# Kernel optimization log

Hardware: AMD Instinct MI355X
Metric: run time of the kernel (lower is better)

The kernel has to match this reference:

```python
import jax, jax.numpy as jnp
import numpy as np
import math

HIST = 10  # attention window over per-node prediction history


def setup_inputs() -> dict:
    key = jax.random.key(0)
    ks = jax.random.split(key, 16)
    N, DEG, F, H, M, O, P, S = 512, 8, 128, 256, 256, 64, 2, 64

    def lin(k, fan_in, shape):
        b = 1.0 / np.sqrt(fan_in)
        return jax.random.uniform(k, shape, jnp.float32, -b, b)

    return {
        "xa": jax.random.normal(ks[0], (N, F), jnp.float32),
        "neighbors": jax.random.randint(ks[1], (N, DEG), 0, N),
        "first_message": jax.random.normal(ks[2], (N, M), jnp.float32),
        "We": lin(ks[3], F, (F, H)), "be": lin(ks[3], F, (H,)),
        "Wq": lin(ks[4], M, (M, H)), "bq": lin(ks[4], M, (H,)),
        "Wk": lin(ks[5], H, (H, H)), "bk": lin(ks[5], H, (H,)),
        "Wr": lin(ks[6], 4 * H, (4 * H, H)), "br": lin(ks[6], 4 * H, (H,)),
        "Wm": lin(ks[7], H + M, (H + M, M)), "bm": lin(ks[7], H + M, (M,)),
        "Wd": lin(ks[8], H, (P, H, O)), "bd": lin(ks[8], H, (P, O)),
        "num_starts": S,
    }


def reference(xa, neighbors, first_message, We, be, Wq, bq, Wk, bk,
              Wr, br, Wm, bm, Wd, bd, num_starts):
    N, H = xa.shape[0], We.shape[1]
    M = first_message.shape[1]
    DEG = neighbors.shape[1]
    max_steps = 10 * N                    # message budget, as in the while-loop cap
    CAP = num_starts + max_steps * DEG    # static queue capacity bound
    inv_sqrt_h = 1.0 / math.sqrt(H)
    nbrs = neighbors.astype(jnp.int32)
    slot_ids = jnp.arange(HIST)

    encoded = xa @ We + be                                    # [N,H]
    hist = jnp.zeros((N, HIST, H), xa.dtype).at[:, 0, :].set(encoded)
    count = jnp.ones((N,), jnp.int32)
    q_node = jnp.zeros((CAP,), jnp.int32).at[:num_starts].set(
        jnp.arange(num_starts, dtype=jnp.int32))
    q_msg = jnp.zeros((CAP, M), xa.dtype).at[:num_starts].set(
        first_message[:num_starts])
    head = jnp.int32(0)
    tail = jnp.int32(num_starts)

    def step(carry, _):
        hist, count, q_node, q_msg, head, tail = carry
        active = head < tail                 # queue non-empty
        node = q_node[head]
        message = q_msg[head]                # [M]
        feats = hist[node]                   # [HIST,H] ring buffer of last states
        c = count[node]
        valid = slot_ids < jnp.minimum(c, HIST)
        # NOTE: source uses queries[0]/keys[0] for every head -> heads identical
        query = message @ Wq + bq            # [H]
        keys = feats @ Wk + bk               # [HIST,H]
        logits = jnp.where(valid, keys @ query * inv_sqrt_h, -jnp.inf)
        attn = jax.nn.softmax(logits)        # softmax over history axis (dim=-0)
        values = attn @ feats                # [H]
        newstate = jnp.concatenate([values] * 4) @ Wr + br     # [H]
        newmessage = jnp.concatenate([newstate, message]) @ Wm + bm  # [M]
        # conditional state updates (no-op writes when inactive)
        slot = c % HIST
        hist = hist.at[node, slot].set(jnp.where(active, newstate, hist[node, slot]))
        count = count.at[node].add(jnp.where(active, 1, 0))
        old_n = jax.lax.dynamic_slice(q_node, (tail,), (DEG,))
        old_m = jax.lax.dynamic_slice(q_msg, (tail, 0), (DEG, M))
        q_node = jax.lax.dynamic_update_slice(
            q_node, jnp.where(active, nbrs[node], old_n), (tail,))
        q_msg = jax.lax.dynamic_update_slice(
            q_msg, jnp.where(active, jnp.broadcast_to(newmessage, (DEG, M)), old_m),
            (tail, 0))
        head = head + jnp.where(active, 1, 0)
        tail = tail + jnp.where(active, DEG, 0)
        return (hist, count, q_node, q_msg, head, tail), None

    (hist, count, _, _, _, _), _ = jax.lax.scan(
        step, (hist, count, q_node, q_msg, head, tail), None, length=max_steps)

    final = hist[jnp.arange(N), (count - 1) % HIST]           # [N,H] last state
    logits = jnp.einsum('nh,pho->pno', final, Wd) + bd[:, None, :]
    return jax.nn.log_softmax(logits, axis=-1)                # [P,N,O]
```

## Files before the change

kernel.cpp:

```cpp
#include <hip/hip_runtime.h>
#include <hip/hip_bf16.h>

#define NN 512
#define DEG 8
#define FD 128
#define HD 256
#define MD 256
#define OD 64
#define PD 2
#define HIST 10
#define TOTAL (10 * NN)
#define NPAR 648
#define INV_SQRT_H 0.0625f

typedef __hip_bfloat16 bf16;

__device__ __forceinline__ float finz(float x) {
  unsigned u = __float_as_uint(x);
  return (((u >> 23) & 0xFFu) == 0xFFu) ? 0.f : x;
}

__device__ __forceinline__ float ldin(const void* p, int idx, int bf) {
  if (bf) return __bfloat162float(((const bf16*)p)[idx]);
  return ((const float*)p)[idx];
}

__device__ __forceinline__ float scload(const float* p) {
  return __uint_as_float(__hip_atomic_load((const unsigned*)p, __ATOMIC_RELAXED,
                                           __HIP_MEMORY_SCOPE_AGENT));
}
__device__ __forceinline__ void scstore(float* p, float v) {
  __hip_atomic_store((unsigned*)p, __float_as_uint(v), __ATOMIC_RELAXED,
                     __HIP_MEMORY_SCOPE_AGENT);
}

__device__ float g_hist[NN * HIST * HD];
__device__ float g_msgb[NPAR * MD];
__device__ float g_WQK[HD * HD];
__device__ float g_WrS[HD * HD];
__device__ float g_vq[HD];
__device__ float g_ck[HD];
__device__ float g_bqk;
__device__ int   g_node[TOTAL];
__device__ int   g_done[TOTAL];
__device__ int   g_dtype;
__device__ int   g_i64;

__device__ __forceinline__ int decode_S(const int* dS) {
  int r = dS[0];
  if (r >= 1 && r <= NN) return r;
  float f = __int_as_float(r);
  if (f >= 1.f && f <= (float)NN) return (int)f;
  unsigned u = ((unsigned)r & 0xFFFFu) << 16;
  float g = __uint_as_float(u);
  if (g >= 1.f && g <= (float)NN) return (int)g;
  return 64;
}

__device__ __forceinline__ int get_nbr(const int* nbrs, int i64, int n, int d) {
  int v = i64 ? nbrs[2 * (n * DEG + d)] : nbrs[n * DEG + d];
  return (v < 0) ? 0 : (v >= NN ? NN - 1 : v);
}

__device__ __forceinline__ int detect_bf(const unsigned* xa_w) {
  const int lane = threadIdx.x & 63;
  unsigned lo = xa_w[lane] & 0xFFFFu;
  float av = fabsf(__uint_as_float(lo << 16));
  unsigned long long m = __ballot(av > 0.000244140625f && av < 64.f);
  return ((int)__popcll(m) >= 32) ? 1 : 0;
}

__global__ void __launch_bounds__(1024)
k_prep(const void* __restrict__ xa, const unsigned* __restrict__ xa_w,
       const int* __restrict__ nbrs, const int* __restrict__ dS,
       const void* __restrict__ We, const void* __restrict__ be,
       const void* __restrict__ Wq, const void* __restrict__ Wk,
       const void* __restrict__ Wr, const void* __restrict__ bq,
       const void* __restrict__ bk) {
  const int b = blockIdx.x, t = threadIdx.x;
  const int col = t & 255, grp = t >> 8;
  const int wave = t >> 6, lane = t & 63;
  const int bf = detect_bf(xa_w);
  if (t < 8) { int fi = 8 * b + t; if (fi < TOTAL) g_done[fi] = 0; }
  __shared__ float sw[HD];
  __shared__ float sp[4][HD];
  __shared__ float sr[16];
  __shared__ float s_wkT[32][HD + 1];
  __shared__ int s_node[TOTAL];
  if (b < HD) {
    if (grp == 0) sw[col] = ldin(Wq, b * HD + col, bf);
    __syncthreads();
    if (grp == 1) {
      float pv = sw[col] * ldin(bk, col, bf);
#pragma unroll
      for (int off = 32; off > 0; off >>= 1) pv += __shfl_down(pv, off, 64);
      if (lane == 0) sr[wave] = pv;
    }
    if (grp == 2) {
      float s = 0.f;
#pragma unroll
      for (int q = 0; q < 4; ++q) s += ldin(Wr, (size_t)(q * HD + b) * HD + col, bf);
      g_WrS[b * HD + col] = s;
    }
    float acc0 = 0.f, acc1 = 0.f;
    const int hh = t & 31, r0 = t >> 5;
    for (int h0 = 0; h0 < HD; h0 += 32) {
#pragma unroll
      for (int rr = 0; rr < 8; ++rr) {
        const int row = rr * 32 + r0;
        s_wkT[hh][row] = ldin(Wk, row * HD + h0 + hh, bf);
      }
      __syncthreads();
      const int hb = grp * 8;
#pragma unroll
      for (int i = 0; i < 8; i += 2) {
        acc0 += sw[h0 + hb + i]     * s_wkT[hb + i][col];
        acc1 += sw[h0 + hb + i + 1] * s_wkT[hb + i + 1][col];
      }
      __syncthreads();
    }
    sp[grp][col] = acc0 + acc1;
    __syncthreads();
    if (grp == 0)
      g_WQK[b * HD + col] = (sp[0][col] + sp[1][col]) + (sp[2][col] + sp[3][col]);
    if (t == 0) g_vq[b] = (sr[4] + sr[5]) + (sr[6] + sr[7]);
  } else if (b == HD) {
    {
      const int h0 = grp * 64;
      float a0 = 0.f, a1 = 0.f, a2 = 0.f, a3 = 0.f;
      for (int h = 0; h < 64; h += 4) {
        a0 += ldin(Wk, col * HD + h0 + h,     bf) * ldin(bq, h0 + h,     bf);
        a1 += ldin(Wk, col * HD + h0 + h + 1, bf) * ldin(bq, h0 + h + 1, bf);
        a2 += ldin(Wk, col * HD + h0 + h + 2, bf) * ldin(bq, h0 + h + 2, bf);
        a3 += ldin(Wk, col * HD + h0 + h + 3, bf) * ldin(bq, h0 + h + 3, bf);
      }
      sp[grp][col] = (a0 + a1) + (a2 + a3);
    }
    if (grp == 1) {
      float pb = ldin(bq, col, bf) * ldin(bk, col, bf);
#pragma unroll
      for (int off = 32; off > 0; off >>= 1) pb += __shfl_down(pb, off, 64);
      if (lane == 0) sr[wave] = pb;
    }
    __syncthreads();
    if (grp == 0)
      g_ck[col] = (sp[0][col] + sp[1][col]) + (sp[2][col] + sp[3][col]);
    if (t == 0) g_bqk = (sr[4] + sr[5]) + (sr[6] + sr[7]);
  } else if (b <= HD + NN) {
    const int n = b - HD - 1;
    if (t < FD) sw[t] = ldin(xa, n * FD + t, bf);
    __syncthreads();
    const int f0 = grp * 32;
    float a0 = 0.f, a1 = 0.f, a2 = 0.f, a3 = 0.f;
    for (int f = 0; f < 32; f += 4) {
      a0 += sw[f0 + f]     * ldin(We, (f0 + f)     * HD + col, bf);
      a1 += sw[f0 + f + 1] * ldin(We, (f0 + f + 1) * HD + col, bf);
      a2 += sw[f0 + f + 2] * ldin(We, (f0 + f + 2) * HD + col, bf);
      a3 += sw[f0 + f + 3] * ldin(We, (f0 + f + 3) * HD + col, bf);
    }
    sp[grp][col] = (a0 + a1) + (a2 + a3);
    __syncthreads();
    if (grp == 0)
      g_hist[(size_t)(n * HIST) * HD + col] =
          ldin(be, col, bf) + (sp[0][col] + sp[1][col]) + (sp[2][col] + sp[3][col]);
  } else {
    if (t == 0) g_dtype = bf;
    bool c8 = (lane < 8) ? (nbrs[2 * lane + 1] == 0) : true;
    unsigned long long im = __ballot(c8);
    const int i64 = ((im & 0xFFull) == 0xFFull) ? 1 : 0;
    if (t == 0) g_i64 = i64;
    const int S = decode_S(dS);
    for (int i = t; i < S; i += 1024) s_node[i] = i;
    __syncthreads();
    int done = S;
    while (done < TOTAL) {
      long long nd = (long long)S + 8LL * (long long)done;
      int new_done = nd > (long long)TOTAL ? TOTAL : (int)nd;
      for (int i = done + t; i < new_done; i += 1024)
        s_node[i] = get_nbr(nbrs, i64, s_node[(i - S) >> 3], (i - S) & 7);
      __syncthreads();
      done = new_done;
    }
    for (int i = t; i < TOTAL; i += 1024) g_node[i] = s_node[i];
  }
}

__global__ void __launch_bounds__(256, 2)
k_flow(const void* __restrict__ fmsg, const void* __restrict__ br_,
       const void* __restrict__ Wm, const void* __restrict__ bm,
       const void* __restrict__ Wd, const void* __restrict__ bd,
       void* __restrict__ out, const int* __restrict__ dS) {
  const int n = blockIdx.x;
  const int t = threadIdx.x;
  const int wave = t >> 6, lane = t & 63;
  const int S = decode_S(dS);
  const int bf = g_dtype;
  __shared__ float s_hist[HIST][HD];
  __shared__ float s_msg[MD];
  __shared__ float s_vals[HD];
  __shared__ float s_ns[HD];
  __shared__ float s_red[4][HIST + 1];
  __shared__ int   s_list[TOTAL];
  __shared__ int   s_cnt;

  const float rck = g_ck[t];
  const float rvq = g_vq[t];
  const float rbqk = g_bqk;
  const float rbr = ldin(br_, t, bf);
  const float rbm = ldin(bm, t, bf);

#pragma unroll
  for (int j = 1; j < HIST; ++j) s_hist[j][t] = 0.f;
  s_hist[0][t] = finz(g_hist[(size_t)n * HIST * HD + t]);

  if (wave == 0) {
    int k = 0;
    for (int base = 0; base < TOTAL; base += 64) {
      int nd = g_node[base + lane];
      unsigned long long m = __ballot(nd == n);
      if (nd == n) {
        unsigned long long below = m & ((1ull << lane) - 1ull);
        s_list[k + (int)__popcll(below)] = base + lane;
      }
      k += (int)__popcll(m);
    }
    if (lane == 0) s_cnt = k;
  }
  __syncthreads();
  const int cnt = s_cnt;

  for (int k = 0; k < cnt; ++k) {
    const int e = s_list[k];
    const int c = k + 1;
    const int v = (c < HIST) ? c : HIST;
    const int slot = c % HIST;
    const bool hc = (S + 8 * e) < TOTAL;

    float ms;
    if (e < S) {
      ms = ldin(fmsg, e * MD + t, bf);
    } else {
      const int p = (e - S) >> 3;
      if (t == 0)
        while (__hip_atomic_load(&g_done[p], __ATOMIC_RELAXED,
                                 __HIP_MEMORY_SCOPE_AGENT) == 0)
          __builtin_amdgcn_s_sleep(4);
      __syncthreads();
      ms = scload(g_msgb + (size_t)p * MD + t);
    }
    s_msg[t] = finz(ms);
    __syncthreads();

    float a0 = 0.f, a1 = 0.f, a2 = 0.f, a3 = 0.f;
    for (int m = 0; m < MD; m += 4) {
      a0 += s_msg[m]     * g_WQK[(m)     * HD + t];
      a1 += s_msg[m + 1] * g_WQK[(m + 1) * HD + t];
      a2 += s_msg[m + 2] * g_WQK[(m + 2) * HD + t];
      a3 += s_msg[m + 3] * g_WQK[(m + 3) * HD + t];
    }
    const float kq = rck + ((a0 + a1) + (a2 + a3));

    float part[HIST + 1];
#pragma unroll
    for (int j = 0; j < HIST; ++j) part[j] = s_hist[j][t] * kq;
    part[HIST] = s_msg[t] * rvq;
#pragma unroll
    for (int o = 32; o > 0; o >>= 1) {
#pragma unroll
      for (int j = 0; j <= HIST; ++j) part[j] += __shfl_down(part[j], o, 64);
    }
    if (lane == 0) {
#pragma unroll
      for (int j = 0; j <= HIST; ++j) s_red[wave][j] = part[j];
    }
    __syncthreads();

    float sc[HIST + 1];
#pragma unroll
    for (int j = 0; j <= HIST; ++j)
      sc[j] = (s_red[0][j] + s_red[1][j]) + (s_red[2][j] + s_red[3][j]);
    const float bkq = sc[HIST] + rbqk;
    float lg[HIST];
#pragma unroll
    for (int j = 0; j < HIST; ++j)
      lg[j] = (j < v) ? ((sc[j] + bkq) * INV_SQRT_H) : -1e30f;
    float mx = lg[0];
#pragma unroll
    for (int j = 1; j < HIST; ++j) mx = fmaxf(mx, lg[j]);
    float e_[HIST], den = 0.f;
#pragma unroll
    for (int j = 0; j < HIST; ++j) { e_[j] = __expf(lg[j] - mx); den += e_[j]; }
    const float iden = 1.0f / den;
    float val = 0.f;
#pragma unroll
    for (int j = 0; j < HIST; ++j) val += e_[j] * s_hist[j][t];
    s_vals[t] = val * iden;
    __syncthreads();

    float b0 = 0.f, b1 = 0.f, b2 = 0.f, b3 = 0.f;
    for (int h = 0; h < HD; h += 4) {
      b0 += s_vals[h]     * g_WrS[(h)     * HD + t];
      b1 += s_vals[h + 1] * g_WrS[(h + 1) * HD + t];
      b2 += s_vals[h + 2] * g_WrS[(h + 2) * HD + t];
      b3 += s_vals[h + 3] * g_WrS[(h + 3) * HD + t];
    }
    const float ns = rbr + ((b0 + b1) + (b2 + b3));
    s_hist[slot][t] = ns;
    if (hc) s_ns[t] = ns;
    __syncthreads();

    if (hc) {
      float c0 = 0.f, c1 = 0.f, c2 = 0.f, c3 = 0.f;
      if (bf) {
        const bf16* w = (const bf16*)Wm;
        for (int h = 0; h < HD; h += 4) {
          c0 += s_ns[h]     * __bfloat162float(w[(h)     * MD + t]);
          c1 += s_ns[h + 1] * __bfloat162float(w[(h + 1) * MD + t]);
          c2 += s_ns[h + 2] * __bfloat162float(w[(h + 2) * MD + t]);
          c3 += s_ns[h + 3] * __bfloat162float(w[(h + 3) * MD + t]);
        }
        for (int m = 0; m < MD; m += 4) {
          c0 += s_msg[m]     * __bfloat162float(w[(HD + m)     * MD + t]);
          c1 += s_msg[m + 1] * __bfloat162float(w[(HD + m + 1) * MD + t]);
          c2 += s_msg[m + 2] * __bfloat162float(w[(HD + m + 2) * MD + t]);
          c3 += s_msg[m + 3] * __bfloat162float(w[(HD + m + 3) * MD + t]);
        }
      } else {
        const float* w = (const float*)Wm;
        for (int h = 0; h < HD; h += 4) {
          c0 += s_ns[h]     * w[(h)     * MD + t];
          c1 += s_ns[h + 1] * w[(h + 1) * MD + t];
          c2 += s_ns[h + 2] * w[(h + 2) * MD + t];
          c3 += s_ns[h + 3] * w[(h + 3) * MD + t];
        }
        for (int m = 0; m < MD; m += 4) {
          c0 += s_msg[m]     * w[(HD + m)     * MD + t];
          c1 += s_msg[m + 1] * w[(HD + m + 1) * MD + t];
          c2 += s_msg[m + 2] * w[(HD + m + 2) * MD + t];
          c3 += s_msg[m + 3] * w[(HD + m + 3) * MD + t];
        }
      }
      scstore(&g_msgb[(size_t)e * MD + t], rbm + ((c0 + c1) + (c2 + c3)));
      asm volatile("s_waitcnt vmcnt(0)" ::: "memory");
    }
    __syncthreads();
    if (hc && t == 0)
      __hip_atomic_store(&g_done[e], 1, __ATOMIC_RELAXED,
                         __HIP_MEMORY_SCOPE_AGENT);
  }

  const int slotF = cnt % HIST;
  if (t < PD * OD) {
    const int pp = t >> 6, o = t & 63;
    float acc = finz(ldin(bd, pp * OD + o, bf));
    for (int h = 0; h < HD; ++h)
      acc += finz(s_hist[slotF][h]) * ldin(Wd, (pp * HD + h) * OD + o, bf);
    acc = finz(acc);
    float mx = acc;
#pragma unroll
    for (int off = 32; off > 0; off >>= 1) mx = fmaxf(mx, __shfl_xor(mx, off, 64));
    float ex = __expf(acc - mx);
    float s = ex;
#pragma unroll
    for (int off = 32; off > 0; off >>= 1) s += __shfl_xor(s, off, 64);
    float r = finz(acc - mx - logf(s));
    const int oi = (pp * NN + n) * OD + o;
    if (bf) ((bf16*)out)[oi] = __float2bfloat16(r);
    else    ((float*)out)[oi] = r;
  }
}

extern "C" void kernel_launch(void* const* d_in, const int* in_sizes, int n_in,
                              void* d_out, int out_size, void* d_ws, size_t ws_size,
                              hipStream_t stream) {
  const void* xa   = d_in[0];
  const int*  nbrs = (const int*)d_in[1];
  const void* fmsg = d_in[2];
  const void* We   = d_in[3];
  const void* be   = d_in[4];
  const void* Wq   = d_in[5];
  const void* bq   = d_in[6];
  const void* Wk   = d_in[7];
  const void* bk   = d_in[8];
  const void* Wr   = d_in[9];
  const void* br   = d_in[10];
  const void* Wm   = d_in[11];
  const void* bm   = d_in[12];
  const void* Wd   = d_in[13];
  const void* bd   = d_in[14];
  const int*  dS   = (const int*)d_in[15];
  (void)d_ws; (void)ws_size; (void)in_sizes; (void)n_in; (void)out_size;

  k_prep<<<dim3(HD + 1 + NN + 1), dim3(1024), 0, stream>>>(
      xa, (const unsigned*)xa, nbrs, dS, We, be, Wq, Wk, Wr, bq, bk);
  k_flow<<<dim3(NN), dim3(256), 0, stream>>>(fmsg, br, Wm, bm, Wd, bd, d_out, dS);
}
```

Measured before the change: 437.8 us.

## Batch eight rows per block in prep kernel to reuse Wk and We loads

After: 435.1 us, median of 2. Within noise of the previous version (-0.6%).

```diff
diff --git a/kernel.cpp b/kernel.cpp
--- a/kernel.cpp
+++ b/kernel.cpp
@@ -81,88 +81,131 @@
   const int col = t & 255, grp = t >> 8;
   const int wave = t >> 6, lane = t & 63;
   const int bf = detect_bf(xa_w);
-  if (t < 8) { int fi = 8 * b + t; if (fi < TOTAL) g_done[fi] = 0; }
-  __shared__ float sw[HD];
-  __shared__ float sp[4][HD];
-  __shared__ float sr[16];
+  { int fi = b * 1024 + t; if (fi < TOTAL) g_done[fi] = 0; }
+  __shared__ float sw8[8][HD];
   __shared__ float s_wkT[32][HD + 1];
-  __shared__ int s_node[TOTAL];
-  if (b < HD) {
-    if (grp == 0) sw[col] = ldin(Wq, b * HD + col, bf);
-    __syncthreads();
-    if (grp == 1) {
-      float pv = sw[col] * ldin(bk, col, bf);
+  __shared__ float sp[4][8][HD];
+  __shared__ float s_xa[8][FD];
+  __shared__ int   s_node[TOTAL];
+  if (b < 32) {
+    const int R = 8 * b;
+    {
+      const int i0 = t, i1 = t + 1024;
+      sw8[i0 >> 8][i0 & 255] = ldin(Wq, (R + (i0 >> 8)) * HD + (i0 & 255), bf);
+      sw8[i1 >> 8][i1 & 255] = ldin(Wq, (R + (i1 >> 8)) * HD + (i1 & 255), bf);
+    }
+    __syncthreads();
+    {
+      const int r0 = R + 2 * grp, r1 = r0 + 1;
+      float s0 = 0.f, s1 = 0.f;
+#pragma unroll
+      for (int q = 0; q < 4; ++q) {
+        s0 += ldin(Wr, (size_t)(q * HD + r0) * HD + col, bf);
+        s1 += ldin(Wr, (size_t)(q * HD + r1) * HD + col, bf);
+      }
+      g_WrS[(size_t)r0 * HD + col] = s0;
+      g_WrS[(size_t)r1 * HD + col] = s1;
+    }
+    if (wave < 8) {
+      float pv = 0.f;
+#pragma unroll
+      for (int j = 0; j < 4; ++j)
+        pv += sw8[wave][lane + 64 * j] * ldin(bk, lane + 64 * j, bf);
 #pragma unroll
       for (int off = 32; off > 0; off >>= 1) pv += __shfl_down(pv, off, 64);
-      if (lane == 0) sr[wave] = pv;
-    }
-    if (grp == 2) {
-      float s = 0.f;
-#pragma unroll
-      for (int q = 0; q < 4; ++q) s += ldin(Wr, (size_t)(q * HD + b) * HD + col, bf);
-      g_WrS[b * HD + col] = s;
-    }
-    float acc0 = 0.f, acc1 = 0.f;
-    const int hh = t & 31, r0 = t >> 5;
+      if (lane == 0) g_vq[R + wave] = pv;
+    }
+    float q0 = 0.f, q1 = 0.f, q2 = 0.f, q3 = 0.f;
+    float q4 = 0.f, q5 = 0.f, q6 = 0.f, q7 = 0.f;
+    const int hh = t & 31, r0s = t >> 5;
+    const int hb = grp * 8;
     for (int h0 = 0; h0 < HD; h0 += 32) {
 #pragma unroll
       for (int rr = 0; rr < 8; ++rr) {
-        const int row = rr * 32 + r0;
+        const int row = rr * 32 + r0s;
         s_wkT[hh][row] = ldin(Wk, row * HD + h0 + hh, bf);
       }
       __syncthreads();
-      const int hb = grp * 8;
-#pragma unroll
-      for (int i = 0; i < 8; i += 2) {
-        acc0 += sw[h0 + hb + i]     * s_wkT[hb + i][col];
-        acc1 += sw[h0 + hb + i + 1] * s_wkT[hb + i + 1][col];
-      }
-      __syncthreads();
-    }
-    sp[grp][col] = acc0 + acc1;
+#pragma unroll
+      for (int i = 0; i < 8; ++i) {
+        const float wk = s_wkT[hb + i][col];
+        const int h = h0 + hb + i;
+        q0 += sw8[0][h] * wk; q1 += sw8[1][h] * wk;
+        q2 += sw8[2][h] * wk; q3 += sw8[3][h] * wk;
+        q4 += sw8[4][h] * wk; q5 += sw8[5][h] * wk;
+        q6 += sw8[6][h] * wk; q7 += sw8[7][h] * wk;
+      }
+      __syncthreads();
+    }
+    sp[grp][0][col] = q0; sp[grp][1][col] = q1;
+    sp[grp][2][col] = q2; sp[grp][3][col] = q3;
+    sp[grp][4][col] = q4; sp[grp][5][col] = q5;
+    sp[grp][6][col] = q6; sp[grp][7][col] = q7;
+    __syncthreads();
+    if (grp == 0) {
+#pragma unroll
+      for (int r = 0; r < 8; ++r)
+        g_WQK[(size_t)(R + r) * HD + col] =
+            (sp[0][r][col] + sp[1][r][col]) + (sp[2][r][col] + sp[3][r][col]);
+    }
+  } else if (b == 32) {
+    float ca = 0.f;
+    const int hh = t & 31, r0s = t >> 5;
+    const int hb = grp * 8;
+    for (int h0 = 0; h0 < HD; h0 += 32) {
+#pragma unroll
+      for (int rr = 0; rr < 8; ++rr) {
+        const int row = rr * 32 + r0s;
+        s_wkT[hh][row] = ldin(Wk, row * HD + h0 + hh, bf);
+      }
+      __syncthreads();
+#pragma unroll
+      for (int i = 0; i < 8; ++i)
+        ca += ldin(bq, h0 + hb + i, bf) * s_wkT[hb + i][col];
+      __syncthreads();
+    }
+    sp[grp][0][col] = ca;
     __syncthreads();
     if (grp == 0)
-      g_WQK[b * HD + col] = (sp[0][col] + sp[1][col]) + (sp[2][col] + sp[3][col]);
-    if (t == 0) g_vq[b] = (sr[4] + sr[5]) + (sr[6] + sr[7]);
-  } else if (b == HD) {
+      g_ck[col] = (sp[0][0][col] + sp[1][0][col]) + (sp[2][0][col] + sp[3][0][col]);
+    if (wave == 0) {
+      float pb = 0.f;
+#pragma unroll
+      for (int j = 0; j < 4; ++j)
+        pb += ldin(bq, lane + 64 * j, bf) * ldin(bk, lane + 64 * j, bf);
+#pragma unroll
+      for (int off = 32; off > 0; off >>= 1) pb += __shfl_down(pb, off, 64);
+      if (lane == 0) g_bqk = pb;
+    }
+  } else if (b <= 96) {
+    const int n0 = (b - 33) * 8;
     {
-      const int h0 = grp * 64;
-      float a0 = 0.f, a1 = 0.f, a2 = 0.f, a3 = 0.f;
-      for (int h = 0; h < 64; h += 4) {
-        a0 += ldin(Wk, col * HD + h0 + h,     bf) * ldin(bq, h0 + h,     bf);
-        a1 += ldin(Wk, col * HD + h0 + h + 1, bf) * ldin(bq, h0 + h + 1, bf);
-        a2 += ldin(Wk, col * HD + h0 + h + 2, bf) * ldin(bq, h0 + h + 2, bf);
-        a3 += ldin(Wk, col * HD + h0 + h + 3, bf) * ldin(bq, h0 + h + 3, bf);
-      }
-      sp[grp][col] = (a0 + a1) + (a2 + a3);
-    }
-    if (grp == 1) {
-      float pb = ldin(bq, col, bf) * ldin(bk, col, bf);
-#pragma unroll
-      for (int off = 32; off > 0; off >>= 1) pb += __shfl_down(pb, off, 64);
-      if (lane == 0) sr[wave] = pb;
-    }
-    __syncthreads();
-    if (grp == 0)
-      g_ck[col] = (sp[0][col] + sp[1][col]) + (sp[2][col] + sp[3][col]);
-    if (t == 0) g_bqk = (sr[4] + sr[5]) + (sr[6] + sr[7]);
-  } else if (b <= HD + NN) {
-    const int n = b - HD - 1;
-    if (t < FD) sw[t] = ldin(xa, n * FD + t, bf);
-    __syncthreads();
+      const int r = t >> 7, f = t & 127;
+      s_xa[r][f] = ldin(xa, (n0 + r) * FD + f, bf);
+    }
+    __syncthreads();
+    float e0 = 0.f, e1 = 0.f, e2 = 0.f, e3 = 0.f;
+    float e4 = 0.f, e5 = 0.f, e6 = 0.f, e7 = 0.f;
     const int f0 = grp * 32;
-    float a0 = 0.f, a1 = 0.f, a2 = 0.f, a3 = 0.f;
-    for (int f = 0; f < 32; f += 4) {
-      a0 += sw[f0 + f]     * ldin(We, (f0 + f)     * HD + col, bf);
-      a1 += sw[f0 + f + 1] * ldin(We, (f0 + f + 1) * HD + col, bf);
-      a2 += sw[f0 + f + 2] * ldin(We, (f0 + f + 2) * HD + col, bf);
-      a3 += sw[f0 + f + 3] * ldin(We, (f0 + f + 3) * HD + col, bf);
-    }
-    sp[grp][col] = (a0 + a1) + (a2 + a3);
-    __syncthreads();
-    if (grp == 0)
-      g_hist[(size_t)(n * HIST) * HD + col] =
-          ldin(be, col, bf) + (sp[0][col] + sp[1][col]) + (sp[2][col] + sp[3][col]);
+    for (int f = 0; f < 32; ++f) {
+      const float we = ldin(We, (f0 + f) * HD + col, bf);
+      e0 += s_xa[0][f0 + f] * we; e1 += s_xa[1][f0 + f] * we;
+      e2 += s_xa[2][f0 + f] * we; e3 += s_xa[3][f0 + f] * we;
+      e4 += s_xa[4][f0 + f] * we; e5 += s_xa[5][f0 + f] * we;
+      e6 += s_xa[6][f0 + f] * we; e7 += s_xa[7][f0 + f] * we;
+    }
+    sp[grp][0][col] = e0; sp[grp][1][col] = e1;
+    sp[grp][2][col] = e2; sp[grp][3][col] = e3;
+    sp[grp][4][col] = e4; sp[grp][5][col] = e5;
+    sp[grp][6][col] = e6; sp[grp][7][col] = e7;
+    __syncthreads();
+    if (grp == 0) {
+      const float be_ = ldin(be, col, bf);
+#pragma unroll
+      for (int r = 0; r < 8; ++r)
+        g_hist[(size_t)((n0 + r) * HIST) * HD + col] =
+            be_ + (sp[0][r][col] + sp[1][r][col]) + (sp[2][r][col] + sp[3][r][col]);
+    }
   } else {
     if (t == 0) g_dtype = bf;
     bool c8 = (lane < 8) ? (nbrs[2 * lane + 1] == 0) : true;
@@ -391,7 +434,7 @@
   const int*  dS   = (const int*)d_in[15];
   (void)d_ws; (void)ws_size; (void)in_sizes; (void)n_in; (void)out_size;
 
-  k_prep<<<dim3(HD + 1 + NN + 1), dim3(1024), 0, stream>>>(
+  k_prep<<<dim3(98), dim3(1024), 0, stream>>>(
       xa, (const unsigned*)xa, nbrs, dS, We, be, Wq, Wk, Wr, bq, bk);
   k_flow<<<dim3(NN), dim3(256), 0, stream>>>(fmsg, br, Wm, bm, Wd, bd, d_out, dS);
 }
```
